# Kernel optimization log

Hardware: AMD Instinct MI355X
Metric: run time of the kernel (lower is better)

## Reference

```python
import jax, jax.numpy as jnp
import numpy as np

KL_W = 0.001
Q_W = 0.1

def setup_inputs() -> dict:
    key = jax.random.key(0)
    k1, k2, k3, k4 = jax.random.split(key, 4)
    B, N, M, L = 2, 4096, 4096, 512
    return {
        'pred': jax.random.normal(k1, (B, N, 3), dtype=jnp.float32),
        'target': jax.random.normal(k2, (B, M, 3), dtype=jnp.float32),
        'mu': jax.random.normal(k3, (B, L), dtype=jnp.float32),
        'logvar': jax.random.normal(k4, (B, L), dtype=jnp.float32),
    }

def reference(pred, target, mu, logvar):
    # Chamfer distance: pairwise squared distances [B, N, M] then min-reductions
    d_pt = jnp.sum((pred[:, :, None, :] - target[:, None, :, :]) ** 2, axis=-1)
    cd = (d_pt.min(axis=2).mean(axis=1) + d_pt.min(axis=1).mean(axis=1)).mean()

    # KL divergence of diagonal Gaussian vs standard normal
    kl = -0.5 * jnp.mean(1.0 + logvar - mu ** 2 - jnp.exp(logvar))

    # Density uniformity: nearest-neighbor self-distance std (unbiased, like torch.std)
    d_pp = jnp.sum((pred[:, :, None, :] - pred[:, None, :, :]) ** 2, axis=-1)
    N = pred.shape[1]
    d_pp = d_pp + jnp.eye(N, dtype=pred.dtype)[None] * 1e6  # mask self-distance
    nn_dist = d_pp.min(axis=2)  # [B, N]
    density = jnp.std(nn_dist, axis=1, ddof=1).mean()

    total = cd + KL_W * kl + Q_W * density
    return total, cd, kl, density
```

## Files before the change

### kernel.cpp

```cpp
#include <hip/hip_runtime.h>
#include <hip/hip_bf16.h>
#include <math.h>

constexpr int B = 2;
constexpr int N = 4096;
constexpr int M = 4096;
constexpr int L = 512;

constexpr float KL_W = 0.001f;
constexpr float Q_W  = 0.1f;

constexpr int THREADS = 256;
constexpr int QPT     = 2;
constexpr int QC      = THREADS * QPT;
constexpr int DT      = 256;
constexpr int GX      = N / QC;
constexpr int GY      = M / DT;
constexpr int GZ      = 3 * B;

constexpr size_t OFF_PARTIAL = 0;
constexpr size_t OFF_BSUMS   = (size_t)GY * GZ * N * 4;

__global__ __launch_bounds__(THREADS) void mgl_pairmin_kernel(
    const float* __restrict__ pred, const float* __restrict__ target,
    float* __restrict__ partial)
{
    __shared__ float4 tile[DT];

    const int z   = blockIdx.z;
    const int dir = z >> 1;
    const int b   = z & 1;

    const float* qb; const float* db;
    if (dir == 0)      { qb = pred   + b * N * 3; db = target + b * M * 3; }
    else if (dir == 1) { qb = target + b * M * 3; db = pred   + b * N * 3; }
    else               { qb = pred   + b * N * 3; db = pred   + b * N * 3; }

    const int q0 = blockIdx.x * QC;
    const int d0 = blockIdx.y * DT;

    {
        const float* p = db + (size_t)(d0 + threadIdx.x) * 3;
        float x = p[0], y = p[1], zz = p[2];
        tile[threadIdx.x] = make_float4(x, y, zz, fmaf(x, x, fmaf(y, y, zz * zz)));
    }

    const int qi0 = q0 + threadIdx.x;
    const int qi1 = qi0 + THREADS;

    const float qx0 = qb[qi0 * 3 + 0], qy0 = qb[qi0 * 3 + 1], qz0 = qb[qi0 * 3 + 2];
    const float qx1 = qb[qi1 * 3 + 0], qy1 = qb[qi1 * 3 + 1], qz1 = qb[qi1 * 3 + 2];
    const float qw0 = fmaf(qx0, qx0, fmaf(qy0, qy0, qz0 * qz0));
    const float qw1 = fmaf(qx1, qx1, fmaf(qy1, qy1, qz1 * qz1));
    const float ax0 = -2.0f * qx0, ay0 = -2.0f * qy0, az0 = -2.0f * qz0;
    const float ax1 = -2.0f * qx1, ay1 = -2.0f * qy1, az1 = -2.0f * qz1;

    __syncthreads();

    float m0 = 3.402823466e+38f;
    float m1 = 3.402823466e+38f;

    if (dir != 2) {
        #pragma unroll 8
        for (int j = 0; j < DT; ++j) {
            float4 t = tile[j];
            float v0 = fmaf(ax0, t.x, fmaf(ay0, t.y, fmaf(az0, t.z, t.w)));
            float v1 = fmaf(ax1, t.x, fmaf(ay1, t.y, fmaf(az1, t.z, t.w)));
            m0 = fminf(m0, v0);
            m1 = fminf(m1, v1);
        }
    } else {
        #pragma unroll 8
        for (int j = 0; j < DT; ++j) {
            float4 t = tile[j];
            const int dj = d0 + j;
            float v0 = fmaf(ax0, t.x, fmaf(ay0, t.y, fmaf(az0, t.z, t.w)));
            float v1 = fmaf(ax1, t.x, fmaf(ay1, t.y, fmaf(az1, t.z, t.w)));
            v0 = (dj == qi0) ? 3.402823466e+38f : v0;
            v1 = (dj == qi1) ? 3.402823466e+38f : v1;
            m0 = fminf(m0, v0);
            m1 = fminf(m1, v1);
        }
    }

    m0 = fmaxf(m0 + qw0, 0.0f);
    m1 = fmaxf(m1 + qw1, 0.0f);

    float* slice = partial + ((size_t)blockIdx.y * GZ + z) * N;
    slice[qi0] = m0;
    slice[qi1] = m1;
}

__global__ __launch_bounds__(256) void mgl_reduce_kernel(
    const float* __restrict__ partial, double* __restrict__ blocksums)
{
    const int tid = threadIdx.x;
    const int bid = blockIdx.x;
    const int z   = bid >> 2;
    const int q4  = ((bid & 3) * 256 + tid) * 4;

    const float4* p = (const float4*)(partial + (size_t)z * N + q4);
    float4 m = p[0];
    #pragma unroll
    for (int gy = 1; gy < GY; ++gy) {
        float4 v = p[(size_t)gy * (GZ * N / 4)];
        m.x = fminf(m.x, v.x); m.y = fminf(m.y, v.y);
        m.z = fminf(m.z, v.z); m.w = fminf(m.w, v.w);
    }

    double s  = (double)m.x + (double)m.y + (double)m.z + (double)m.w;
    double ss = (double)m.x * m.x + (double)m.y * m.y
              + (double)m.z * m.z + (double)m.w * m.w;

    #pragma unroll
    for (int off = 32; off > 0; off >>= 1) {
        s  += __shfl_down(s,  off, 64);
        ss += __shfl_down(ss, off, 64);
    }
    __shared__ double wred[4][2];
    const int wid  = tid >> 6;
    const int lane = tid & 63;
    if (lane == 0) { wred[wid][0] = s; wred[wid][1] = ss; }
    __syncthreads();
    if (tid == 0) {
        double ts = wred[0][0] + wred[1][0] + wred[2][0] + wred[3][0];
        double tss = wred[0][1] + wred[1][1] + wred[2][1] + wred[3][1];
        blocksums[bid * 2 + 0] = ts;
        blocksums[bid * 2 + 1] = tss;
    }
}

__global__ __launch_bounds__(256) void mgl_final_kernel(
    const double* __restrict__ blocksums, const float* __restrict__ mu,
    const float* __restrict__ logvar, float* __restrict__ out)
{
    const int tid = threadIdx.x;

    double skl = 0.0;
    #pragma unroll
    for (int k = 0; k < 4; ++k) {
        int i = tid * 4 + k;
        double m  = (double)mu[i];
        double lv = (double)logvar[i];
        skl += 1.0 + lv - m * m - exp(lv);
    }
    #pragma unroll
    for (int off = 32; off > 0; off >>= 1)
        skl += __shfl_down(skl, off, 64);

    __shared__ double wkl[4];
    const int wid  = tid >> 6;
    const int lane = tid & 63;
    if (lane == 0) wkl[wid] = skl;
    __syncthreads();

    if (tid == 0) {
        double tkl = wkl[0] + wkl[1] + wkl[2] + wkl[3];

        double sPT[B] = {0.0, 0.0}, sTP[B] = {0.0, 0.0};
        double sPP[B] = {0.0, 0.0}, ssPP[B] = {0.0, 0.0};
        for (int bid = 0; bid < 24; ++bid) {
            const int z   = bid >> 2;
            const int dir = z >> 1;
            const int bb  = z & 1;
            double s  = blocksums[bid * 2 + 0];
            double ss = blocksums[bid * 2 + 1];
            if (dir == 0)      sPT[bb] += s;
            else if (dir == 1) sTP[bb] += s;
            else             { sPP[bb] += s; ssPP[bb] += ss; }
        }

        double cd = 0.0;
        #pragma unroll
        for (int bb = 0; bb < B; ++bb)
            cd += sPT[bb] / (double)N + sTP[bb] / (double)M;
        cd /= (double)B;

        double density = 0.0;
        #pragma unroll
        for (int bb = 0; bb < B; ++bb) {
            double s  = sPP[bb];
            double ss = ssPP[bb];
            double var = (ss - s * s / (double)N) / (double)(N - 1);
            density += sqrt(var > 0.0 ? var : 0.0);
        }
        density /= (double)B;

        double kl = -0.5 * tkl / (double)(B * L);

        double total = cd + (double)KL_W * kl + (double)Q_W * density;
        out[0] = (float)total;
        out[1] = (float)cd;
        out[2] = (float)kl;
        out[3] = (float)density;
    }
}

extern "C" void kernel_launch(void* const* d_in, const int* in_sizes, int n_in,
                              void* d_out, int out_size, void* d_ws, size_t ws_size,
                              hipStream_t stream) {
    const float* pred   = (const float*)d_in[0];
    const float* target = (const float*)d_in[1];
    const float* mu     = (const float*)d_in[2];
    const float* logvar = (const float*)d_in[3];
    float* out = (float*)d_out;

    char* ws = (char*)d_ws;
    float*  partial   = (float*)(ws + OFF_PARTIAL);
    double* blocksums = (double*)(ws + OFF_BSUMS);

    mgl_pairmin_kernel<<<dim3(GX, GY, GZ), THREADS, 0, stream>>>(pred, target, partial);
    mgl_reduce_kernel<<<24, 256, 0, stream>>>(partial, blocksums);
    mgl_final_kernel<<<1, 256, 0, stream>>>(blocksums, mu, logvar, out);
}
```

Baseline: 75.17 us.

## Fuse final reduction into reduce kernel via last-block atomic counter

Removes the third kernel launch by having the last reduce block, detected with an atomic counter that the pairmin kernel resets, compute KL and the final outputs. It also changes the query mapping so each thread handles two adjacent points instead of points strided by the block size, and raises the inner-loop unroll from 8 to 16. The intent is to save one launch's overhead and gap. The risks are uncoalesced query loads and extra registers from the larger unroll.

```diff
diff --git a/kernel.cpp b/kernel.cpp
--- a/kernel.cpp
+++ b/kernel.cpp
@@ -18,14 +18,20 @@
 constexpr int GY      = M / DT;
 constexpr int GZ      = 3 * B;
 
+constexpr int RBLOCKS = 24;
+
 constexpr size_t OFF_PARTIAL = 0;
 constexpr size_t OFF_BSUMS   = (size_t)GY * GZ * N * 4;
+constexpr size_t OFF_CNT     = OFF_BSUMS + RBLOCKS * 2 * 8;
 
 __global__ __launch_bounds__(THREADS) void mgl_pairmin_kernel(
     const float* __restrict__ pred, const float* __restrict__ target,
-    float* __restrict__ partial)
+    float* __restrict__ partial, unsigned* __restrict__ counter)
 {
     __shared__ float4 tile[DT];
+
+    if (blockIdx.x == 0 && blockIdx.y == 0 && blockIdx.z == 0 && threadIdx.x == 0)
+        *counter = 0u;
 
     const int z   = blockIdx.z;
     const int dir = z >> 1;
@@ -45,8 +51,8 @@
         tile[threadIdx.x] = make_float4(x, y, zz, fmaf(x, x, fmaf(y, y, zz * zz)));
     }
 
-    const int qi0 = q0 + threadIdx.x;
-    const int qi1 = qi0 + THREADS;
+    const int qi0 = q0 + threadIdx.x * 2;
+    const int qi1 = qi0 + 1;
 
     const float qx0 = qb[qi0 * 3 + 0], qy0 = qb[qi0 * 3 + 1], qz0 = qb[qi0 * 3 + 2];
     const float qx1 = qb[qi1 * 3 + 0], qy1 = qb[qi1 * 3 + 1], qz1 = qb[qi1 * 3 + 2];
@@ -61,7 +67,7 @@
     float m1 = 3.402823466e+38f;
 
     if (dir != 2) {
-        #pragma unroll 8
+        #pragma unroll 16
         for (int j = 0; j < DT; ++j) {
             float4 t = tile[j];
             float v0 = fmaf(ax0, t.x, fmaf(ay0, t.y, fmaf(az0, t.z, t.w)));
@@ -70,7 +76,7 @@
             m1 = fminf(m1, v1);
         }
     } else {
-        #pragma unroll 8
+        #pragma unroll 16
         for (int j = 0; j < DT; ++j) {
             float4 t = tile[j];
             const int dj = d0 + j;
@@ -92,7 +98,10 @@
 }
 
 __global__ __launch_bounds__(256) void mgl_reduce_kernel(
-    const float* __restrict__ partial, double* __restrict__ blocksums)
+    const float* __restrict__ partial, double* __restrict__ blocksums,
+    unsigned* __restrict__ counter,
+    const float* __restrict__ mu, const float* __restrict__ logvar,
+    float* __restrict__ out)
 {
     const int tid = threadIdx.x;
     const int bid = blockIdx.x;
@@ -123,34 +132,31 @@
     if (lane == 0) { wred[wid][0] = s; wred[wid][1] = ss; }
     __syncthreads();
     if (tid == 0) {
-        double ts = wred[0][0] + wred[1][0] + wred[2][0] + wred[3][0];
+        double ts  = wred[0][0] + wred[1][0] + wred[2][0] + wred[3][0];
         double tss = wred[0][1] + wred[1][1] + wred[2][1] + wred[3][1];
         blocksums[bid * 2 + 0] = ts;
         blocksums[bid * 2 + 1] = tss;
     }
-}
-
-__global__ __launch_bounds__(256) void mgl_final_kernel(
-    const double* __restrict__ blocksums, const float* __restrict__ mu,
-    const float* __restrict__ logvar, float* __restrict__ out)
-{
-    const int tid = threadIdx.x;
+
+    __threadfence();
+    __shared__ int is_last;
+    if (tid == 0)
+        is_last = (atomicAdd(counter, 1u) == (unsigned)(RBLOCKS - 1)) ? 1 : 0;
+    __syncthreads();
+    if (!is_last) return;
 
     double skl = 0.0;
     #pragma unroll
     for (int k = 0; k < 4; ++k) {
         int i = tid * 4 + k;
-        double m  = (double)mu[i];
+        double mm = (double)mu[i];
         double lv = (double)logvar[i];
-        skl += 1.0 + lv - m * m - exp(lv);
+        skl += 1.0 + lv - mm * mm - exp(lv);
     }
     #pragma unroll
     for (int off = 32; off > 0; off >>= 1)
         skl += __shfl_down(skl, off, 64);
-
     __shared__ double wkl[4];
-    const int wid  = tid >> 6;
-    const int lane = tid & 63;
     if (lane == 0) wkl[wid] = skl;
     __syncthreads();
 
@@ -159,15 +165,23 @@
 
         double sPT[B] = {0.0, 0.0}, sTP[B] = {0.0, 0.0};
         double sPP[B] = {0.0, 0.0}, ssPP[B] = {0.0, 0.0};
-        for (int bid = 0; bid < 24; ++bid) {
-            const int z   = bid >> 2;
-            const int dir = z >> 1;
-            const int bb  = z & 1;
-            double s  = blocksums[bid * 2 + 0];
-            double ss = blocksums[bid * 2 + 1];
-            if (dir == 0)      sPT[bb] += s;
-            else if (dir == 1) sTP[bb] += s;
-            else             { sPP[bb] += s; ssPP[bb] += ss; }
+        for (int k = 0; k < RBLOCKS; ++k) {
+            const int zz  = k >> 2;
+            const int dr  = zz >> 1;
+            const int bb  = zz & 1;
+            double bs, bss;
+            if (k == bid) { bs = blocksums[k*2+0]; bss = blocksums[k*2+1]; }
+            else {
+                unsigned long long u0 = __hip_atomic_load((unsigned long long*)&blocksums[k*2+0],
+                                            __ATOMIC_RELAXED, __HIP_MEMORY_SCOPE_AGENT);
+                unsigned long long u1 = __hip_atomic_load((unsigned long long*)&blocksums[k*2+1],
+                                            __ATOMIC_RELAXED, __HIP_MEMORY_SCOPE_AGENT);
+                bs  = __longlong_as_double((long long)u0);
+                bss = __longlong_as_double((long long)u1);
+            }
+            if (dr == 0)      sPT[bb] += bs;
+            else if (dr == 1) sTP[bb] += bs;
+            else            { sPP[bb] += bs; ssPP[bb] += bss; }
         }
 
         double cd = 0.0;
@@ -179,9 +193,9 @@
         double density = 0.0;
         #pragma unroll
         for (int bb = 0; bb < B; ++bb) {
-            double s  = sPP[bb];
-            double ss = ssPP[bb];
-            double var = (ss - s * s / (double)N) / (double)(N - 1);
+            double sv  = sPP[bb];
+            double ssv = ssPP[bb];
+            double var = (ssv - sv * sv / (double)N) / (double)(N - 1);
             density += sqrt(var > 0.0 ? var : 0.0);
         }
         density /= (double)B;
@@ -206,10 +220,10 @@
     float* out = (float*)d_out;
 
     char* ws = (char*)d_ws;
-    float*  partial   = (float*)(ws + OFF_PARTIAL);
-    double* blocksums = (double*)(ws + OFF_BSUMS);
-
-    mgl_pairmin_kernel<<<dim3(GX, GY, GZ), THREADS, 0, stream>>>(pred, target, partial);
-    mgl_reduce_kernel<<<24, 256, 0, stream>>>(partial, blocksums);
-    mgl_final_kernel<<<1, 256, 0, stream>>>(blocksums, mu, logvar, out);
+    float*    partial   = (float*)(ws + OFF_PARTIAL);
+    double*   blocksums = (double*)(ws + OFF_BSUMS);
+    unsigned* counter   = (unsigned*)(ws + OFF_CNT);
+
+    mgl_pairmin_kernel<<<dim3(GX, GY, GZ), THREADS, 0, stream>>>(pred, target, partial, counter);
+    mgl_reduce_kernel<<<RBLOCKS, 256, 0, stream>>>(partial, blocksums, counter, mu, logvar, out);
 }
```

After: 78.67 us. 4.7% more time.
